# Performance work log

Hardware: AMD Instinct MI355X
Metric: run time of the kernel (lower is better)

The kernel has to match this reference:

```python
import jax, jax.numpy as jnp
import numpy as np

N_NODES = 100000
N_EDGES = 3200000
N_GRAPHS = 2048


def setup_inputs() -> dict:
    key = jax.random.key(0)
    ks = jax.random.split(key, 6)
    x = jax.random.normal(ks[0], (N_NODES, 5), dtype=jnp.float32)
    edge_index = jax.random.randint(ks[1], (2, N_EDGES), 0, N_NODES, dtype=jnp.int64)
    batch = jnp.sort(jax.random.randint(ks[2], (N_NODES,), 0, N_GRAPHS, dtype=jnp.int64))
    # Glorot-ish init for GCN weights
    W1 = jax.random.normal(ks[3], (5, 30), dtype=jnp.float32) * (1.0 / np.sqrt(5.0))
    b1 = jnp.zeros((30,), dtype=jnp.float32)
    W2 = jax.random.normal(ks[4], (30, 8), dtype=jnp.float32) * (1.0 / np.sqrt(30.0))
    b2 = jnp.zeros((8,), dtype=jnp.float32)
    return {"x": x, "edge_index": edge_index, "batch": batch,
            "W1": W1, "b1": b1, "W2": W2, "b2": b2}


def _gcn_conv(x, src, dst, W, b, n_nodes):
    # PyG GCNConv: linear transform, then D^-1/2 A_hat D^-1/2 aggregation (self-loops included in src/dst).
    h = x @ W                                              # [N, out]
    deg = jax.ops.segment_sum(jnp.ones_like(dst, dtype=h.dtype), dst, num_segments=n_nodes)
    dinv = jnp.where(deg > 0, deg ** -0.5, 0.0)            # [N]
    norm = dinv[src] * dinv[dst]                           # [E+N]
    msg = h[src] * norm[:, None]                           # gather + scale
    out = jax.ops.segment_sum(msg, dst, num_segments=n_nodes)  # scatter-add
    return out + b


def reference(x, edge_index, batch, W1, b1, W2, b2):
    n = x.shape[0]
    loops = jnp.arange(n, dtype=edge_index.dtype)
    src = jnp.concatenate([edge_index[0], loops])          # add self-loops
    dst = jnp.concatenate([edge_index[1], loops])

    h = _gcn_conv(x, src, dst, W1, b1, n)
    h = jax.nn.relu(h)
    # F.dropout with training=False (eval mode) is identity
    h = _gcn_conv(h, src, dst, W2, b2, n)                   # [N, 8]

    # scatter_mean over graph ids
    sums = jax.ops.segment_sum(h, batch, num_segments=N_GRAPHS)          # [G, 8]
    counts = jax.ops.segment_sum(jnp.ones((n,), dtype=h.dtype), batch, num_segments=N_GRAPHS)
    return sums / jnp.maximum(counts, 1.0)[:, None]
```

## Files before the change

### kernel.cpp

```cpp
#include <hip/hip_runtime.h>

#define N_NODES 100000
#define N_EDGES 3200000
#define N_GRAPHS 2048
#define BSH 6
#define BSZ 64
#define NB 1563
#define FILL_BLOCKS 512
#define CHUNK 6250

__device__ __forceinline__ void gAtomAdd(float* p, float v) { unsafeAtomicAdd(p, v); }

__global__ void k_count(const int* __restrict__ dst, int* __restrict__ bcnt,
                        int* __restrict__ blockBase) {
  __shared__ int hist[NB];
  int tid = threadIdx.x, blk = blockIdx.x;
  for (int i = tid; i < NB; i += 256) hist[i] = 0;
  __syncthreads();
  int beg = blk * CHUNK, end = beg + CHUNK;
  for (int e = beg + tid; e < end; e += 256) atomicAdd(&hist[dst[e] >> BSH], 1);
  __syncthreads();
  for (int i = tid; i < NB; i += 256) {
    int h = hist[i];
    if (h) blockBase[blk * NB + i] = atomicAdd(&bcnt[i], h);
  }
}

__global__ void k_bscan(const int* __restrict__ bcnt, int* __restrict__ boffs) {
  __shared__ int sh[512];
  __shared__ int carry;
  int tid = threadIdx.x;
  if (tid == 0) carry = 0;
  __syncthreads();
  for (int c = 0; c < NB; c += 512) {
    int i = c + tid;
    int v = (i < NB) ? bcnt[i] : 0;
    sh[tid] = v;
    __syncthreads();
    for (int off = 1; off < 512; off <<= 1) {
      int t = (tid >= off) ? sh[tid - off] : 0;
      __syncthreads();
      sh[tid] += t;
      __syncthreads();
    }
    if (i < NB) boffs[i] = carry + sh[tid] - v;
    __syncthreads();
    if (tid == 511) carry += sh[511];
    __syncthreads();
  }
  if (tid == 0) boffs[NB] = N_EDGES;
}

__global__ void k_fill(const int* __restrict__ src, const int* __restrict__ dst,
                       const int* __restrict__ boffs, const int* __restrict__ blockBase,
                       unsigned* __restrict__ stage1) {
  __shared__ int lbase[NB];
  int tid = threadIdx.x, blk = blockIdx.x;
  for (int i = tid; i < NB; i += 256) lbase[i] = boffs[i] + blockBase[blk * NB + i];
  __syncthreads();
  int beg = blk * CHUNK, end = beg + CHUNK;
  for (int e = beg + tid; e < end; e += 256) {
    int d = dst[e], s = src[e];
    int pos = atomicAdd(&lbase[d >> BSH], 1);
    stage1[pos] = ((unsigned)s << BSH) | (unsigned)(d & (BSZ - 1));
  }
}

__global__ void k_prep2(const unsigned* __restrict__ stage1, const int* __restrict__ boffs,
                        const float* __restrict__ x, int* __restrict__ noffs,
                        float* __restrict__ dinv, float* __restrict__ xd8) {
  __shared__ int cnt[BSZ];
  __shared__ int sc[BSZ];
  int b = blockIdx.x, tid = threadIdx.x;
  if (tid < BSZ) cnt[tid] = 0;
  __syncthreads();
  int beg = boffs[b], end = boffs[b + 1];
  for (int k = beg + tid; k < end; k += 256) atomicAdd(&cnt[stage1[k] & (BSZ - 1)], 1);
  __syncthreads();
  if (tid < BSZ) sc[tid] = cnt[tid];
  __syncthreads();
  for (int off = 1; off < BSZ; off <<= 1) {
    int t = (tid < BSZ && tid >= off) ? sc[tid - off] : 0;
    __syncthreads();
    if (tid < BSZ) sc[tid] += t;
    __syncthreads();
  }
  if (tid < BSZ) {
    int node = b * BSZ + tid;
    if (node <= N_NODES) noffs[node] = beg + sc[tid] - cnt[tid];
    if (node < N_NODES) {
      float di = rsqrtf((float)(cnt[tid] + 1));
      dinv[node] = di;
      float r[5];
#pragma unroll
      for (int c = 0; c < 5; c++) r[c] = x[node * 5 + c] * di;
      float4* xv = (float4*)xd8;
      xv[node * 2]     = make_float4(r[0], r[1], r[2], r[3]);
      xv[node * 2 + 1] = make_float4(r[4], 0.f, 0.f, 0.f);
    }
  }
}

__global__ void k_fill2(const unsigned* __restrict__ stage1, const int* __restrict__ boffs,
                        const int* __restrict__ noffs, int* __restrict__ csr) {
  __shared__ int curs[BSZ];
  int b = blockIdx.x, tid = threadIdx.x;
  if (tid < BSZ) {
    int node = b * BSZ + tid;
    curs[tid] = (node < N_NODES) ? noffs[node] : N_EDGES;
  }
  __syncthreads();
  int beg = boffs[b], end = boffs[b + 1];
  for (int k = beg + tid; k < end; k += 256) {
    unsigned u = stage1[k];
    int pos = atomicAdd(&curs[u & (BSZ - 1)], 1);
    csr[pos] = (int)(u >> BSH);
  }
}

__global__ void k_agg1(const int* __restrict__ csr, const int* __restrict__ noffs,
                       const float* __restrict__ xd8, const float* __restrict__ dinv,
                       const float* __restrict__ W1, const float* __restrict__ b1,
                       const float* __restrict__ W2, float* __restrict__ g2) {
  __shared__ float w1[150], bb1[30], w2[240];
  int tid = threadIdx.x;
  for (int i = tid; i < 150; i += 256) w1[i] = W1[i];
  for (int i = tid; i < 30; i += 256) bb1[i] = b1[i];
  for (int i = tid; i < 240; i += 256) w2[i] = W2[i];
  __syncthreads();
  int n = blockIdx.x * 256 + tid;
  if (n >= N_NODES) return;
  const float4* xv = (const float4*)xd8;
  float a0 = 0, a1 = 0, a2 = 0, a3 = 0, a4 = 0;
  int k = noffs[n], end = noffs[n + 1];
  for (; k + 4 <= end; k += 4) {
    int s0 = csr[k], s1 = csr[k + 1], s2 = csr[k + 2], s3 = csr[k + 3];
    float4 q0 = xv[s0 * 2], q1 = xv[s1 * 2], q2 = xv[s2 * 2], q3 = xv[s3 * 2];
    float c0 = xd8[s0 * 8 + 4], c1 = xd8[s1 * 8 + 4], c2 = xd8[s2 * 8 + 4], c3 = xd8[s3 * 8 + 4];
    a0 += q0.x + q1.x + q2.x + q3.x;
    a1 += q0.y + q1.y + q2.y + q3.y;
    a2 += q0.z + q1.z + q2.z + q3.z;
    a3 += q0.w + q1.w + q2.w + q3.w;
    a4 += c0 + c1 + c2 + c3;
  }
  for (; k < end; k++) {
    int s = csr[k];
    float4 q = xv[s * 2];
    a0 += q.x; a1 += q.y; a2 += q.z; a3 += q.w; a4 += xd8[s * 8 + 4];
  }
  float di = dinv[n];
  float t[5] = {(a0 + xd8[n * 8 + 0]) * di, (a1 + xd8[n * 8 + 1]) * di,
                (a2 + xd8[n * 8 + 2]) * di, (a3 + xd8[n * 8 + 3]) * di,
                (a4 + xd8[n * 8 + 4]) * di};
  float h[30];
#pragma unroll
  for (int j = 0; j < 30; j++) h[j] = bb1[j];
#pragma unroll
  for (int kk = 0; kk < 5; kk++)
#pragma unroll
    for (int j = 0; j < 30; j++) h[j] += t[kk] * w1[kk * 30 + j];
  float g[8] = {0, 0, 0, 0, 0, 0, 0, 0};
#pragma unroll
  for (int j = 0; j < 30; j++) {
    float hj = fmaxf(h[j], 0.f);
#pragma unroll
    for (int c = 0; c < 8; c++) g[c] += hj * w2[j * 8 + c];
  }
  float4* gv = (float4*)g2;
  gv[n * 2]     = make_float4(g[0] * di, g[1] * di, g[2] * di, g[3] * di);
  gv[n * 2 + 1] = make_float4(g[4] * di, g[5] * di, g[6] * di, g[7] * di);
}

__global__ void k_agg2(const int* __restrict__ csr, const int* __restrict__ noffs,
                       const float* __restrict__ g2, const float* __restrict__ dinv,
                       const float* __restrict__ b2, const int* __restrict__ batch,
                       float* __restrict__ gsum) {
  __shared__ float gpool[64 * 8];
  __shared__ float bb2[8];
  __shared__ int batch0s;
  int blk = blockIdx.x, tid = threadIdx.x;
  for (int i = tid; i < 64 * 8; i += 256) gpool[i] = 0.f;
  if (tid < 8) bb2[tid] = b2[tid];
  if (tid == 0) {
    int n0 = blk * 256;
    batch0s = batch[n0 < N_NODES ? n0 : (N_NODES - 1)];
  }
  __syncthreads();
  int n = blk * 256 + tid;
  int batch0 = batch0s;
  if (n < N_NODES) {
    const float4* gv = (const float4*)g2;
    float4 lo = make_float4(0, 0, 0, 0), hi = make_float4(0, 0, 0, 0);
    int k = noffs[n], end = noffs[n + 1];
    for (; k + 2 <= end; k += 2) {
      int s0 = csr[k], s1 = csr[k + 1];
      float4 p0 = gv[s0 * 2], q0 = gv[s0 * 2 + 1];
      float4 p1 = gv[s1 * 2], q1 = gv[s1 * 2 + 1];
      lo.x += p0.x + p1.x; lo.y += p0.y + p1.y;
      lo.z += p0.z + p1.z; lo.w += p0.w + p1.w;
      hi.x += q0.x + q1.x; hi.y += q0.y + q1.y;
      hi.z += q0.z + q1.z; hi.w += q0.w + q1.w;
    }
    for (; k < end; k++) {
      int s = csr[k];
      float4 p = gv[s * 2], q = gv[s * 2 + 1];
      lo.x += p.x; lo.y += p.y; lo.z += p.z; lo.w += p.w;
      hi.x += q.x; hi.y += q.y; hi.z += q.z; hi.w += q.w;
    }
    float di = dinv[n];
    float4 sl = gv[n * 2], sh = gv[n * 2 + 1];
    float val[8] = {di * (lo.x + sl.x) + bb2[0], di * (lo.y + sl.y) + bb2[1],
                    di * (lo.z + sl.z) + bb2[2], di * (lo.w + sl.w) + bb2[3],
                    di * (hi.x + sh.x) + bb2[4], di * (hi.y + sh.y) + bb2[5],
                    di * (hi.z + sh.z) + bb2[6], di * (hi.w + sh.w) + bb2[7]};
    int gid = batch[n], goff = gid - batch0;
#pragma unroll
    for (int c = 0; c < 8; c++) {
      if (goff < 64) atomicAdd(&gpool[goff * 8 + c], val[c]);
      else           gAtomAdd(&gsum[gid * 8 + c], val[c]);
    }
  }
  __syncthreads();
  for (int i = tid; i < 64 * 8; i += 256) {
    int gid = batch0 + (i >> 3);
    float v = gpool[i];
    if (gid < N_GRAPHS && v != 0.f) gAtomAdd(&gsum[gid * 8 + (i & 7)], v);
  }
}

__global__ void k_final(const float* __restrict__ gsum, const int* __restrict__ batch,
                        float* __restrict__ out) {
  int i = blockIdx.x * 256 + threadIdx.x;
  if (i >= N_GRAPHS * 8) return;
  int g = i >> 3;
  int lo = 0, hi = N_NODES;
  while (lo < hi) { int m = (lo + hi) >> 1; if (batch[m] < g) lo = m + 1; else hi = m; }
  int lo2 = lo, hi2 = N_NODES;
  while (lo2 < hi2) { int m = (lo2 + hi2) >> 1; if (batch[m] <= g) lo2 = m + 1; else hi2 = m; }
  float c = (float)(lo2 - lo);
  out[i] = gsum[i] / fmaxf(c, 1.f);
}

extern "C" void kernel_launch(void* const* d_in, const int* in_sizes, int n_in,
                              void* d_out, int out_size, void* d_ws, size_t ws_size,
                              hipStream_t stream) {
  const float* x    = (const float*)d_in[0];
  const int* ei     = (const int*)d_in[1];
  const int* batch  = (const int*)d_in[2];
  const float* W1   = (const float*)d_in[3];
  const float* b1   = (const float*)d_in[4];
  const float* W2   = (const float*)d_in[5];
  const float* b2   = (const float*)d_in[6];
  const int* srcp = ei;
  const int* dstp = ei + N_EDGES;
  float* out = (float*)d_out;

  char* base = (char*)d_ws;
  size_t o = 0;
  auto carve = [&](size_t bytes) -> char* {
    char* p = base + o;
    o += (bytes + 255) & ~(size_t)255;
    return p;
  };
  int* bcnt        = (int*)carve((size_t)NB * 4);
  int* boffs       = (int*)carve((size_t)(NB + 1) * 4);
  int* blockBase   = (int*)carve((size_t)FILL_BLOCKS * NB * 4);
  unsigned* stage1 = (unsigned*)carve((size_t)N_EDGES * 4);
  int* csr         = (int*)carve((size_t)N_EDGES * 4);
  int* noffs       = (int*)carve((size_t)(N_NODES + 2) * 4);
  float* dinv      = (float*)carve((size_t)N_NODES * 4);
  float* xd8       = (float*)carve((size_t)N_NODES * 8 * 4);
  float* g2        = (float*)carve((size_t)N_NODES * 8 * 4);
  float* gsum      = (float*)carve((size_t)N_GRAPHS * 8 * 4);

  hipMemsetAsync(bcnt, 0, (size_t)NB * 4, stream);
  hipMemsetAsync(gsum, 0, (size_t)N_GRAPHS * 8 * 4, stream);

  k_count<<<FILL_BLOCKS, 256, 0, stream>>>(dstp, bcnt, blockBase);
  k_bscan<<<1, 512, 0, stream>>>(bcnt, boffs);
  k_fill<<<FILL_BLOCKS, 256, 0, stream>>>(srcp, dstp, boffs, blockBase, stage1);
  k_prep2<<<NB, 256, 0, stream>>>(stage1, boffs, x, noffs, dinv, xd8);
  k_fill2<<<NB, 256, 0, stream>>>(stage1, boffs, noffs, csr);
  k_agg1<<<(N_NODES + 255) / 256, 256, 0, stream>>>(csr, noffs, xd8, dinv, W1, b1, W2, g2);
  k_agg2<<<(N_NODES + 255) / 256, 256, 0, stream>>>(csr, noffs, g2, dinv, b2, batch, gsum);
  k_final<<<64, 256, 0, stream>>>(gsum, batch, out);
}
```

Baseline: 210.7 us.

## Use 256-node superbuckets and fuse CSR prep and fill into one kernel

Widens the first-pass bucket size from 64 to 256 nodes, so there are 391 buckets instead of 1563. This shrinks the blockBase matrix and lets the bucket scan finish in one pass. The per-node count/scan/dinv/xd8 kernel and the second CSR fill kernel become one kernel that re-reads the bucket's stage slice from cache, saving a launch and a noffs round trip. The cost is fewer, larger blocks in the fused kernel (391 blocks, about 8K edges each) and more contention on 256 shared-memory counters.

```diff
diff --git a/kernel.cpp b/kernel.cpp
--- a/kernel.cpp
+++ b/kernel.cpp
@@ -3,118 +3,98 @@
 #define N_NODES 100000
 #define N_EDGES 3200000
 #define N_GRAPHS 2048
-#define BSH 6
-#define BSZ 64
-#define NB 1563
+#define SSH 8
+#define SSZ 256
+#define NSB 391
 #define FILL_BLOCKS 512
 #define CHUNK 6250
 
 __device__ __forceinline__ void gAtomAdd(float* p, float v) { unsafeAtomicAdd(p, v); }
 
-__global__ void k_count(const int* __restrict__ dst, int* __restrict__ bcnt,
-                        int* __restrict__ blockBase) {
-  __shared__ int hist[NB];
+__global__ void kA_count(const int* __restrict__ dst, int* __restrict__ bcnt,
+                         int* __restrict__ blockBase) {
+  __shared__ int hist[NSB];
   int tid = threadIdx.x, blk = blockIdx.x;
-  for (int i = tid; i < NB; i += 256) hist[i] = 0;
+  for (int i = tid; i < NSB; i += 256) hist[i] = 0;
   __syncthreads();
   int beg = blk * CHUNK, end = beg + CHUNK;
-  for (int e = beg + tid; e < end; e += 256) atomicAdd(&hist[dst[e] >> BSH], 1);
-  __syncthreads();
-  for (int i = tid; i < NB; i += 256) {
+  for (int e = beg + tid; e < end; e += 256) atomicAdd(&hist[dst[e] >> SSH], 1);
+  __syncthreads();
+  for (int i = tid; i < NSB; i += 256) {
     int h = hist[i];
-    if (h) blockBase[blk * NB + i] = atomicAdd(&bcnt[i], h);
-  }
-}
-
-__global__ void k_bscan(const int* __restrict__ bcnt, int* __restrict__ boffs) {
+    if (h) blockBase[blk * NSB + i] = atomicAdd(&bcnt[i], h);
+  }
+}
+
+__global__ void k_bscan(const int* __restrict__ bcnt, int* __restrict__ sboffs) {
   __shared__ int sh[512];
-  __shared__ int carry;
   int tid = threadIdx.x;
-  if (tid == 0) carry = 0;
-  __syncthreads();
-  for (int c = 0; c < NB; c += 512) {
-    int i = c + tid;
-    int v = (i < NB) ? bcnt[i] : 0;
-    sh[tid] = v;
-    __syncthreads();
-    for (int off = 1; off < 512; off <<= 1) {
-      int t = (tid >= off) ? sh[tid - off] : 0;
-      __syncthreads();
-      sh[tid] += t;
-      __syncthreads();
-    }
-    if (i < NB) boffs[i] = carry + sh[tid] - v;
-    __syncthreads();
-    if (tid == 511) carry += sh[511];
-    __syncthreads();
-  }
-  if (tid == 0) boffs[NB] = N_EDGES;
-}
-
-__global__ void k_fill(const int* __restrict__ src, const int* __restrict__ dst,
-                       const int* __restrict__ boffs, const int* __restrict__ blockBase,
-                       unsigned* __restrict__ stage1) {
-  __shared__ int lbase[NB];
+  int v = (tid < NSB) ? bcnt[tid] : 0;
+  sh[tid] = v;
+  __syncthreads();
+  for (int off = 1; off < 512; off <<= 1) {
+    int t = (tid >= off) ? sh[tid - off] : 0;
+    __syncthreads();
+    sh[tid] += t;
+    __syncthreads();
+  }
+  if (tid < NSB) sboffs[tid] = sh[tid] - v;
+  if (tid == 0) sboffs[NSB] = N_EDGES;
+}
+
+__global__ void kB_fill(const int* __restrict__ src, const int* __restrict__ dst,
+                        const int* __restrict__ sboffs, const int* __restrict__ blockBase,
+                        unsigned* __restrict__ stage) {
+  __shared__ int lbase[NSB];
   int tid = threadIdx.x, blk = blockIdx.x;
-  for (int i = tid; i < NB; i += 256) lbase[i] = boffs[i] + blockBase[blk * NB + i];
+  for (int i = tid; i < NSB; i += 256) lbase[i] = sboffs[i] + blockBase[blk * NSB + i];
   __syncthreads();
   int beg = blk * CHUNK, end = beg + CHUNK;
   for (int e = beg + tid; e < end; e += 256) {
     int d = dst[e], s = src[e];
-    int pos = atomicAdd(&lbase[d >> BSH], 1);
-    stage1[pos] = ((unsigned)s << BSH) | (unsigned)(d & (BSZ - 1));
-  }
-}
-
-__global__ void k_prep2(const unsigned* __restrict__ stage1, const int* __restrict__ boffs,
-                        const float* __restrict__ x, int* __restrict__ noffs,
-                        float* __restrict__ dinv, float* __restrict__ xd8) {
-  __shared__ int cnt[BSZ];
-  __shared__ int sc[BSZ];
+    int pos = atomicAdd(&lbase[d >> SSH], 1);
+    stage[pos] = ((unsigned)s << SSH) | (unsigned)(d & (SSZ - 1));
+  }
+}
+
+__global__ void kC_csr(const unsigned* __restrict__ stage, const int* __restrict__ sboffs,
+                       const float* __restrict__ x, int* __restrict__ noffs,
+                       float* __restrict__ dinv, float* __restrict__ xd8,
+                       int* __restrict__ csr) {
+  __shared__ int cnt[SSZ], sc[SSZ], cur[SSZ];
   int b = blockIdx.x, tid = threadIdx.x;
-  if (tid < BSZ) cnt[tid] = 0;
-  __syncthreads();
-  int beg = boffs[b], end = boffs[b + 1];
-  for (int k = beg + tid; k < end; k += 256) atomicAdd(&cnt[stage1[k] & (BSZ - 1)], 1);
-  __syncthreads();
-  if (tid < BSZ) sc[tid] = cnt[tid];
-  __syncthreads();
-  for (int off = 1; off < BSZ; off <<= 1) {
-    int t = (tid < BSZ && tid >= off) ? sc[tid - off] : 0;
-    __syncthreads();
-    if (tid < BSZ) sc[tid] += t;
-    __syncthreads();
-  }
-  if (tid < BSZ) {
-    int node = b * BSZ + tid;
-    if (node <= N_NODES) noffs[node] = beg + sc[tid] - cnt[tid];
-    if (node < N_NODES) {
-      float di = rsqrtf((float)(cnt[tid] + 1));
-      dinv[node] = di;
-      float r[5];
-#pragma unroll
-      for (int c = 0; c < 5; c++) r[c] = x[node * 5 + c] * di;
-      float4* xv = (float4*)xd8;
-      xv[node * 2]     = make_float4(r[0], r[1], r[2], r[3]);
-      xv[node * 2 + 1] = make_float4(r[4], 0.f, 0.f, 0.f);
-    }
-  }
-}
-
-__global__ void k_fill2(const unsigned* __restrict__ stage1, const int* __restrict__ boffs,
-                        const int* __restrict__ noffs, int* __restrict__ csr) {
-  __shared__ int curs[BSZ];
-  int b = blockIdx.x, tid = threadIdx.x;
-  if (tid < BSZ) {
-    int node = b * BSZ + tid;
-    curs[tid] = (node < N_NODES) ? noffs[node] : N_EDGES;
-  }
-  __syncthreads();
-  int beg = boffs[b], end = boffs[b + 1];
+  cnt[tid] = 0;
+  __syncthreads();
+  int beg = sboffs[b], end = sboffs[b + 1];
+  for (int k = beg + tid; k < end; k += 256) atomicAdd(&cnt[stage[k] & (SSZ - 1)], 1);
+  __syncthreads();
+  sc[tid] = cnt[tid];
+  __syncthreads();
+  for (int off = 1; off < SSZ; off <<= 1) {
+    int t = (tid >= off) ? sc[tid - off] : 0;
+    __syncthreads();
+    sc[tid] += t;
+    __syncthreads();
+  }
+  int excl = sc[tid] - cnt[tid];
+  int node = b * SSZ + tid;
+  if (node <= N_NODES) noffs[node] = beg + excl;
+  if (node < N_NODES) {
+    float di = rsqrtf((float)(cnt[tid] + 1));
+    dinv[node] = di;
+    float r[5];
+#pragma unroll
+    for (int c = 0; c < 5; c++) r[c] = x[node * 5 + c] * di;
+    float4* xv = (float4*)xd8;
+    xv[node * 2]     = make_float4(r[0], r[1], r[2], r[3]);
+    xv[node * 2 + 1] = make_float4(r[4], 0.f, 0.f, 0.f);
+  }
+  cur[tid] = beg + excl;
+  __syncthreads();
   for (int k = beg + tid; k < end; k += 256) {
-    unsigned u = stage1[k];
-    int pos = atomicAdd(&curs[u & (BSZ - 1)], 1);
-    csr[pos] = (int)(u >> BSH);
+    unsigned u = stage[k];
+    int pos = atomicAdd(&cur[u & (SSZ - 1)], 1);
+    csr[pos] = (int)(u >> SSH);
   }
 }
 
@@ -262,10 +242,10 @@
     o += (bytes + 255) & ~(size_t)255;
     return p;
   };
-  int* bcnt        = (int*)carve((size_t)NB * 4);
-  int* boffs       = (int*)carve((size_t)(NB + 1) * 4);
-  int* blockBase   = (int*)carve((size_t)FILL_BLOCKS * NB * 4);
-  unsigned* stage1 = (unsigned*)carve((size_t)N_EDGES * 4);
+  int* bcnt        = (int*)carve((size_t)NSB * 4);
+  int* sboffs      = (int*)carve((size_t)(NSB + 1) * 4);
+  int* blockBase   = (int*)carve((size_t)FILL_BLOCKS * NSB * 4);
+  unsigned* stage  = (unsigned*)carve((size_t)N_EDGES * 4);
   int* csr         = (int*)carve((size_t)N_EDGES * 4);
   int* noffs       = (int*)carve((size_t)(N_NODES + 2) * 4);
   float* dinv      = (float*)carve((size_t)N_NODES * 4);
@@ -273,14 +253,13 @@
   float* g2        = (float*)carve((size_t)N_NODES * 8 * 4);
   float* gsum      = (float*)carve((size_t)N_GRAPHS * 8 * 4);
 
-  hipMemsetAsync(bcnt, 0, (size_t)NB * 4, stream);
+  hipMemsetAsync(bcnt, 0, (size_t)NSB * 4, stream);
   hipMemsetAsync(gsum, 0, (size_t)N_GRAPHS * 8 * 4, stream);
 
-  k_count<<<FILL_BLOCKS, 256, 0, stream>>>(dstp, bcnt, blockBase);
-  k_bscan<<<1, 512, 0, stream>>>(bcnt, boffs);
-  k_fill<<<FILL_BLOCKS, 256, 0, stream>>>(srcp, dstp, boffs, blockBase, stage1);
-  k_prep2<<<NB, 256, 0, stream>>>(stage1, boffs, x, noffs, dinv, xd8);
-  k_fill2<<<NB, 256, 0, stream>>>(stage1, boffs, noffs, csr);
+  kA_count<<<FILL_BLOCKS, 256, 0, stream>>>(dstp, bcnt, blockBase);
+  k_bscan<<<1, 512, 0, stream>>>(bcnt, sboffs);
+  kB_fill<<<FILL_BLOCKS, 256, 0, stream>>>(srcp, dstp, sboffs, blockBase, stage);
+  kC_csr<<<NSB, 256, 0, stream>>>(stage, sboffs, x, noffs, dinv, xd8, csr);
   k_agg1<<<(N_NODES + 255) / 256, 256, 0, stream>>>(csr, noffs, xd8, dinv, W1, b1, W2, g2);
   k_agg2<<<(N_NODES + 255) / 256, 256, 0, stream>>>(csr, noffs, g2, dinv, b2, batch, gsum);
   k_final<<<64, 256, 0, stream>>>(gsum, batch, out);
```

After: 194.8 us. 1.08x faster.
